# Kernel optimization log

Hardware: AMD Instinct MI355X
Metric: run time of the kernel (lower is better)

## Reference

```python
import jax, jax.numpy as jnp
import numpy as np

NUM_CLIP_VIT_FEAT = 576  # default kwarg of mixed_mask


def _mixed_mask(pad_ends, full_starts, full_ends, bt2i, blm, B, S):
    # Faithful translation of OmniAttentionMechanism.mixed_mask evaluated over
    # all (b, q_idx, kv_idx). Note python operator precedence: & binds tighter
    # than ^, so the original expression is (A&t2i) ^ (B&C&lm) ^ (D&mmu).
    q_idx = jnp.arange(S)[:, None]          # [S,1]
    kv_idx = jnp.arange(S)[None, :]         # [1,S]
    causal_qk = q_idx >= kv_idx             # [S,S]
    # kv_idx < pad_ends[b, kv_idx]  ->  arange(S) < pad_ends  (per batch row)
    pad_region = jnp.arange(S) < pad_ends   # [B,S] over kv
    causal = (~pad_region)[:, None, :] & causal_qk[None]              # [B,S,S]
    # full block: kv in [full_starts[q], full_ends[q])
    full = (kv_idx < full_ends[:, None]) & (kv_idx >= full_starts[:, None])  # [S,S]
    eye = q_idx == kv_idx                                             # [S,S]
    t2i = eye[None] ^ (causal | full[None])                           # [B,S,S]
    lm = causal_qk                                                    # [S,S]
    mmu = causal_qk | (kv_idx <= NUM_CLIP_VIT_FEAT + 3)               # [S,S]
    b = jnp.arange(B)[:, None, None]
    mask = ((b < bt2i) & t2i) \
         ^ ((b >= bt2i) & (b < bt2i + blm) & lm[None]) \
         ^ ((b >= bt2i + blm) & mmu[None])
    return mask  # [B,S,S] bool


def setup_inputs() -> dict:
    key = jax.random.key(0)
    B_T2I, B_LM, B_MMU = 4, 4, 4
    B, H, S, D = B_T2I + B_LM + B_MMU, 8, 1024, 64
    k1, k2, k3 = jax.random.split(key, 3)
    q = jax.random.normal(k1, (B, H, S, D), jnp.float32)
    k = jax.random.normal(k2, (B, H, S, D), jnp.float32)
    v = jax.random.normal(k3, (B, H, S, D), jnp.float32)

    # full_starts/full_ends from image_begin_ends=[(512,1024)]
    full_starts = np.arange(S)
    full_ends = np.arange(S)
    for ib, ie in [(512, 1024)]:
        full_starts[ib:ie] = ib
        full_ends[ib:ie] = ie

    # pad_ends from default pad_begin_ends=[(0,256),(0,300),(0,400),(0,0)]
    pad_ends = np.tile(np.arange(S), (B, 1))
    for cnt, (pb, pe) in enumerate([(0, 256), (0, 300), (0, 400), (0, 0)]):
        pad_ends[cnt, pb:pe] = pe

    return {
        "q": q, "k": k, "v": v,
        "pad_ends": jnp.asarray(pad_ends, jnp.int32),
        "full_starts": jnp.asarray(full_starts, jnp.int32),
        "full_ends": jnp.asarray(full_ends, jnp.int32),
        "batch_size_t2i": B_T2I,
        "batch_size_lm": B_LM,
    }


def reference(q, k, v, pad_ends, full_starts, full_ends, batch_size_t2i, batch_size_lm):
    B, H, S, D = q.shape
    mask = _mixed_mask(pad_ends, full_starts, full_ends,
                       batch_size_t2i, batch_size_lm, B, S)      # [B,S,S]
    scale = 1.0 / jnp.sqrt(jnp.asarray(D, q.dtype))
    scores = jnp.einsum('bhqd,bhkd->bhqk', q, k) * scale          # [B,H,S,S]
    scores = jnp.where(mask[:, None], scores, jnp.asarray(-1e30, scores.dtype))
    attn = jax.nn.softmax(scores, axis=-1)
    return jnp.einsum('bhqk,bhkd->bhqd', attn, v)
```

## Files before the change

kernel.cpp:

```cpp
#include <hip/hip_runtime.h>


typedef __attribute__((ext_vector_type(8))) short short8;
typedef __attribute__((ext_vector_type(4))) float floatx4;
typedef __attribute__((ext_vector_type(4))) unsigned int uint4v;

#define S_LEN 1024
#define D_DIM 64
#define H_NUM 8
#define B_NUM 12
#define BT2I_CONST 4
#define BLM_CONST 4
#define NUM_CLIP_P3 579
#define KV_ELEMS (B_NUM * H_NUM * S_LEN * D_DIM)
#define P_EPS 7.888609052210118e-31f

__device__ __forceinline__ float bf2f(short s) {
    unsigned int u = ((unsigned int)(unsigned short)s) << 16;
    return __builtin_bit_cast(float, u);
}
__device__ __forceinline__ short f2bf(float f) {
    unsigned int u = __builtin_bit_cast(unsigned int, f);
    unsigned int r = (u + 0x7fffu + ((u >> 16) & 1u)) >> 16;
    return (short)(unsigned short)r;
}
__device__ __forceinline__ short scale_bf(short x) {
    float f = bf2f(x) * 0.125f;
    return (short)(unsigned short)(__builtin_bit_cast(unsigned int, f) >> 16);
}
__device__ __forceinline__ int detect_bf16(const unsigned int* q) {
    int l = threadIdx.x & 63;
    unsigned int w = q[l];
    unsigned int e = (w >> 7) & 0xffu;
    bool sane = (e >= 100u && e <= 140u);
    unsigned long long m = __ballot(sane);
    return (__popcll(m) > 32) ? 1 : 0;
}

__global__ __launch_bounds__(256)
void preprocess_kv(const void* __restrict__ Kv, const void* __restrict__ Vv,
                   const unsigned int* __restrict__ Qw,
                   short* __restrict__ Kf, short* __restrict__ Vf) {
    __shared__ __align__(16) short Ls[64][72];
    const int is_bf16 = detect_bf16(Qw);
    const int x = blockIdx.x;
    const int kind = x & 1;
    const int kt = (x >> 1) & 15;
    const int bh = x >> 5;
    const int t = threadIdx.x;
    const long long base = (long long)bh * S_LEN * D_DIM + (long long)kt * 64 * D_DIM;
    const void* Src = kind ? Vv : Kv;

    #pragma unroll
    for (int j = 0; j < 4; ++j) {
        int lin = j * 1024 + t * 4;
        int row = lin >> 6, col = lin & 63;
        long long src = base + (long long)row * D_DIM + col;
        if (is_bf16) {
            const short* p = (const short*)Src + src;
            Ls[row][col] = p[0]; Ls[row][col + 1] = p[1];
            Ls[row][col + 2] = p[2]; Ls[row][col + 3] = p[3];
        } else {
            floatx4 f = *(const floatx4*)((const float*)Src + src);
            Ls[row][col] = f2bf(f[0]); Ls[row][col + 1] = f2bf(f[1]);
            Ls[row][col + 2] = f2bf(f[2]); Ls[row][col + 3] = f2bf(f[3]);
        }
    }
    __syncthreads();

    short* dst = (kind ? Vf : Kf) + ((long long)bh * 16 + kt) * 4096;
    if (kind == 0) {
        #pragma unroll
        for (int rep = 0; rep < 2; ++rep) {
            int idx = rep * 256 + t;
            int fh = idx >> 6, lam = idx & 63;
            int f = fh >> 1, hh = fh & 1, q = lam >> 4, l16 = lam & 15;
            short8 v = *(const short8*)&Ls[f * 16 + l16][hh * 32 + q * 8];
            *(short8*)(dst + (fh * 64 + lam) * 8) = v;
        }
    } else {
        #pragma unroll
        for (int rep = 0; rep < 2; ++rep) {
            int idx = rep * 256 + t;
            int ch = idx >> 6, lam = idx & 63;
            int c = ch >> 1, hh = ch & 1, q = lam >> 4, l16 = lam & 15;
            short tmp[8];
            #pragma unroll
            for (int j = 0; j < 8; ++j) tmp[j] = Ls[hh * 32 + q * 8 + j][c * 16 + l16];
            *(short8*)(dst + (ch * 64 + lam) * 8) = *(short8*)tmp;
        }
    }
}

__global__ __launch_bounds__(256, 2)
void omni_attn_main(const void* __restrict__ Qv, const int* __restrict__ pad_ends,
                    const int* __restrict__ fstarts, const int* __restrict__ fends,
                    const short* __restrict__ Kf, const short* __restrict__ Vf,
                    float* __restrict__ Out) {
    __shared__ unsigned int padbits[32];

    const int lid = blockIdx.x;
    const int h = lid & 7;
    const int perm = lid >> 3;
    const int b = perm >> 3;
    const int j = perm & 7;
    const int lpt[8] = {7, 0, 6, 1, 5, 2, 4, 3};
    const int qtb = lpt[j];
    const int qb0 = qtb * 128;

    const int t = threadIdx.x;
    const int wq = t >> 6;
    const int l = t & 63;
    const int lane16 = l & 15;
    const int quad = l >> 4;

    const int is_bf16 = detect_bf16((const unsigned int*)Qv);
    const int cls = (b < BT2I_CONST) ? 0 : ((b < BT2I_CONST + BLM_CONST) ? 1 : 2);
    const int bh = b * H_NUM + h;
    const long long base = (long long)bh * S_LEN * D_DIM;

    #pragma unroll
    for (int kk2 = 0; kk2 < 4; ++kk2) {
        int k = kk2 * 256 + t;
        bool nonpad = (k >= pad_ends[b * S_LEN + k]);
        unsigned long long m = __ballot(nonpad);
        if (l == 0) {
            int widx = kk2 * 8 + wq * 2;
            padbits[widx]     = (unsigned int)m;
            padbits[widx + 1] = (unsigned int)(m >> 32);
        }
    }
    __syncthreads();

    int fs_min, fe_max, fnp;
    {
        int fsv = min(fstarts[qb0 + l], fstarts[qb0 + 64 + l]);
        int fev = max(fends[qb0 + l],   fends[qb0 + 64 + l]);
        unsigned int word = 0u;
        if (l < 32) word = padbits[l];
        int pos = word ? (l * 32 + __builtin_ctz(word)) : 0x7fffffff;
        #pragma unroll
        for (int off = 1; off < 64; off <<= 1) {
            fsv = min(fsv, __shfl_xor(fsv, off, 64));
            fev = max(fev, __shfl_xor(fev, off, 64));
            pos = min(pos, __shfl_xor(pos, off, 64));
        }
        fs_min = fsv; fe_max = fev; fnp = pos;
    }
    const int qmax_blk = qb0 + 127;
    const bool risky = (cls == 0) && (fnp >= qb0) && (fnp <= qmax_blk);

    unsigned int keepmask = 0u;
    #pragma unroll
    for (int kt = 0; kt < 16; ++kt) {
        const int kvbase = kt * 64;
        const unsigned int w0 = padbits[kt * 2], w1 = padbits[kt * 2 + 1];
        bool keep;
        if (cls == 0) {
            bool allpad = (w0 | w1) == 0u;
            keep = risky ||
                   ((kvbase < fe_max) && (kvbase + 64 > fs_min)) ||
                   ((kvbase <= qmax_blk) && (!allpad || (kvbase >= qb0)));
        } else if (cls == 1) {
            keep = (kvbase <= qmax_blk);
        } else {
            keep = (kvbase <= qmax_blk) || (kvbase <= NUM_CLIP_P3);
        }
        keepmask |= (keep ? 1u : 0u) << kt;
    }

    short8 aq[2][2];
    #pragma unroll
    for (int rb = 0; rb < 2; ++rb) {
        const int row = qb0 + wq * 32 + rb * 16 + lane16;
        if (is_bf16) {
            const short8* qp = (const short8*)((const short*)Qv + base
                                               + (long long)row * D_DIM + quad * 8);
            short8 r0 = qp[0], r1 = qp[4];
            #pragma unroll
            for (int jj = 0; jj < 8; ++jj) {
                aq[rb][0][jj] = scale_bf(r0[jj]);
                aq[rb][1][jj] = scale_bf(r1[jj]);
            }
        } else {
            const floatx4* qp = (const floatx4*)((const float*)Qv + base
                                                 + (long long)row * D_DIM + quad * 8);
            floatx4 f0 = qp[0], f1 = qp[1], f2 = qp[8], f3 = qp[9];
            #pragma unroll
            for (int jj = 0; jj < 4; ++jj) {
                aq[rb][0][jj]     = f2bf(f0[jj] * 0.125f);
                aq[rb][0][4 + jj] = f2bf(f1[jj] * 0.125f);
                aq[rb][1][jj]     = f2bf(f2[jj] * 0.125f);
                aq[rb][1][4 + jj] = f2bf(f3[jj] * 0.125f);
            }
        }
    }

    int qvl[2], fsl[2], fel[2], fsmax[2], femin[2];
    #pragma unroll
    for (int rb = 0; rb < 2; ++rb) {
        qvl[rb] = qb0 + wq * 32 + rb * 16 + lane16;
        fsl[rb] = fstarts[qvl[rb]];
        fel[rb] = fends[qvl[rb]];
        int a = fsl[rb], e = fel[rb];
        #pragma unroll
        for (int off = 1; off < 16; off <<= 1) {
            a = max(a, __shfl_xor(a, off, 64));
            e = min(e, __shfl_xor(e, off, 64));
        }
        fsmax[rb] = a; femin[rb] = e;
    }

    floatx4 Oc[2][4];
    float lsum[2] = {0.f, 0.f};
    #pragma unroll
    for (int rb = 0; rb < 2; ++rb)
        #pragma unroll
        for (int c = 0; c < 4; ++c) Oc[rb][c] = (floatx4){0.f, 0.f, 0.f, 0.f};

    const short* Kfb = Kf + (long long)bh * (16 * 4096);
    const short* Vfb = Vf + (long long)bh * (16 * 4096);

    short8 kkf[4][2];
    short8 vvf[4][2];

    auto load_K = [&](int kt) {
        const short8* p = (const short8*)(Kfb + (long long)kt * 4096);
        #pragma unroll
        for (int f = 0; f < 4; ++f)
            #pragma unroll
            for (int hh = 0; hh < 2; ++hh)
                kkf[f][hh] = p[(f * 2 + hh) * 64 + l];
    };
    auto load_V = [&](int kt) {
        const short8* p = (const short8*)(Vfb + (long long)kt * 4096);
        #pragma unroll
        for (int c = 0; c < 4; ++c)
            #pragma unroll
            for (int hh = 0; hh < 2; ++hh)
                vvf[c][hh] = p[(c * 2 + hh) * 64 + l];
    };

    unsigned int mrem = keepmask;
    int kt = __builtin_ctz(mrem); mrem &= mrem - 1;
    load_K(kt); load_V(kt);
    for (;;) {
        int ktN = -1;
        if (mrem) { ktN = __builtin_ctz(mrem); mrem &= mrem - 1; }

        const int kvbase = kt * 64;
        const unsigned int w0c = padbits[kt * 2], w1c = padbits[kt * 2 + 1];

        short8 pa[2][2];
        #pragma unroll
        for (int rb = 0; rb < 2; ++rb) {
            floatx4 sc[4];
            #pragma unroll
            for (int f = 0; f < 4; ++f) {
                floatx4 c = (floatx4){0.f, 0.f, 0.f, 0.f};
                c = __builtin_amdgcn_mfma_f32_16x16x32_bf16(kkf[f][0], aq[rb][0], c, 0, 0, 0);
                c = __builtin_amdgcn_mfma_f32_16x16x32_bf16(kkf[f][1], aq[rb][1], c, 0, 0, 0);
                sc[f] = c;
            }
            const int qlo = qb0 + wq * 32 + rb * 16;
            bool fast;
            if (cls == 0) {
                bool np_all  = ((w0c & w1c) == 0xffffffffu);
                bool below   = (kvbase + 63 < qlo);
                bool eyefree = below || (kvbase > qlo + 15);
                fast = (np_all && below) ||
                       (eyefree && (kvbase >= fsmax[rb]) && (kvbase + 64 <= femin[rb]));
            } else if (cls == 1) {
                fast = (kvbase + 63 <= qlo);
            } else {
                fast = (kvbase + 63 <= qlo) || (kvbase + 63 <= NUM_CLIP_P3);
            }
            if (!fast) {
                const int q = qvl[rb];
                #pragma unroll
                for (int f = 0; f < 4; ++f) {
                    const unsigned int word = (f < 2) ? w0c : w1c;
                    const int sh = 16 * (f & 1) + 4 * quad;
                    #pragma unroll
                    for (int r = 0; r < 4; ++r) {
                        const int k = kvbase + f * 16 + 4 * quad + r;
                        bool m;
                        if (cls == 0) {
                            bool knp    = ((word >> (sh + r)) & 1u) != 0u;
                            bool causal = knp && (q >= k);
                            bool full   = (k >= fsl[rb]) && (k < fel[rb]);
                            m = (q == k) != (causal || full);
                        } else if (cls == 1) {
                            m = (q >= k);
                        } else {
                            m = (q >= k) || (k <= NUM_CLIP_P3);
                        }
                        sc[f][r] = m ? sc[f][r] : -1e30f;
                    }
                }
            }
            unsigned int uu[4][2];
            float ls = 0.f;
            #pragma unroll
            for (int f = 0; f < 4; ++f) {
                float p0 = __expf(sc[f][0]) + P_EPS;
                float p1 = __expf(sc[f][1]) + P_EPS;
                float p2 = __expf(sc[f][2]) + P_EPS;
                float p3 = __expf(sc[f][3]) + P_EPS;
                ls += p0 + p1 + p2 + p3;
                asm("v_cvt_pk_bf16_f32 %0, %1, %2" : "=v"(uu[f][0]) : "v"(p0), "v"(p1));
                asm("v_cvt_pk_bf16_f32 %0, %1, %2" : "=v"(uu[f][1]) : "v"(p2), "v"(p3));
            }
            lsum[rb] += ls;
            #pragma unroll
            for (int hh = 0; hh < 2; ++hh) {
                unsigned int x0 = uu[2 * hh][0],     y0 = uu[2 * hh + 1][0];
                unsigned int x1 = uu[2 * hh][1],     y1 = uu[2 * hh + 1][1];
                asm("v_permlane32_swap_b32 %0, %1" : "+v"(x0), "+v"(y0));
                asm("v_permlane16_swap_b32 %0, %1" : "+v"(x0), "+v"(y0));
                asm("v_permlane32_swap_b32 %0, %1" : "+v"(x1), "+v"(y1));
                asm("v_permlane16_swap_b32 %0, %1" : "+v"(x1), "+v"(y1));
                uint4v w;
                w[0] = x0; w[1] = x1; w[2] = y0; w[3] = y1;
                pa[rb][hh] = __builtin_bit_cast(short8, w);
            }
        }

        if (ktN >= 0) load_K(ktN);

        #pragma unroll
        for (int c = 0; c < 4; ++c) {
            Oc[0][c] = __builtin_amdgcn_mfma_f32_16x16x32_bf16(pa[0][0], vvf[c][0], Oc[0][c], 0, 0, 0);
            Oc[0][c] = __builtin_amdgcn_mfma_f32_16x16x32_bf16(pa[0][1], vvf[c][1], Oc[0][c], 0, 0, 0);
            Oc[1][c] = __builtin_amdgcn_mfma_f32_16x16x32_bf16(pa[1][0], vvf[c][0], Oc[1][c], 0, 0, 0);
            Oc[1][c] = __builtin_amdgcn_mfma_f32_16x16x32_bf16(pa[1][1], vvf[c][1], Oc[1][c], 0, 0, 0);
        }

        if (ktN >= 0) load_V(ktN);
        if (ktN < 0) break;
        kt = ktN;
    }

    #pragma unroll
    for (int rb = 0; rb < 2; ++rb) {
        float s = lsum[rb];
        s += __shfl_xor(s, 16, 64);
        s += __shfl_xor(s, 32, 64);
        float* ob = Out + ((long long)bh * S_LEN + qb0 + wq * 32 + rb * 16) * D_DIM;
        #pragma unroll
        for (int r = 0; r < 4; ++r) {
            float sv = __shfl(s, quad * 4 + r, 64);
            float inv = 1.0f / sv;
            #pragma unroll
            for (int c = 0; c < 4; ++c)
                ob[(quad * 4 + r) * D_DIM + c * 16 + lane16] = Oc[rb][c][r] * inv;
        }
    }
}

__global__ __launch_bounds__(256)
void omni_attn_fallback(const void* __restrict__ Qv, const void* __restrict__ Kv,
                        const void* __restrict__ Vv, const int* __restrict__ pad_ends,
                        const int* __restrict__ fstarts, const int* __restrict__ fends,
                        float* __restrict__ Out) {
    __shared__ short Ks[64][72];
    __shared__ short Vts[64][72];
    __shared__ short Ps[4][16][72];
    __shared__ int   padv[64];
    const int qt = blockIdx.x, h = blockIdx.y, b = blockIdx.z;
    const int t = threadIdx.x, wq = t >> 6, l = t & 63;
    const int lane16 = l & 15, quad = l >> 4;
    const int is_bf16 = detect_bf16((const unsigned int*)Qv);
    const int cls = (b < BT2I_CONST) ? 0 : ((b < BT2I_CONST + BLM_CONST) ? 1 : 2);
    const int bh = b * H_NUM + h;
    const long long base = (long long)bh * S_LEN * D_DIM;
    const short* Kb16 = (const short*)Kv + base;
    const short* Vb16 = (const short*)Vv + base;
    const float* Kbf = (const float*)Kv + base;
    const float* Vbf = (const float*)Vv + base;
    const int qbase = qt * 64 + wq * 16;
    short8 aq0, aq1;
    if (is_bf16) {
        const short8* qp = (const short8*)((const short*)Qv + base + (qbase + lane16) * D_DIM + quad * 8);
        short8 r0 = qp[0], r1 = qp[4];
        #pragma unroll
        for (int jj = 0; jj < 8; ++jj) { aq0[jj] = scale_bf(r0[jj]); aq1[jj] = scale_bf(r1[jj]); }
    } else {
        const floatx4* qp = (const floatx4*)((const float*)Qv + base + (qbase + lane16) * D_DIM + quad * 8);
        floatx4 f0 = qp[0], f1 = qp[1], f2 = qp[8], f3 = qp[9];
        #pragma unroll
        for (int jj = 0; jj < 4; ++jj) {
            aq0[jj] = f2bf(f0[jj] * 0.125f); aq0[4 + jj] = f2bf(f1[jj] * 0.125f);
            aq1[jj] = f2bf(f2[jj] * 0.125f); aq1[4 + jj] = f2bf(f3[jj] * 0.125f);
        }
    }
    int qg[4], fs[4], fe[4];
    #pragma unroll
    for (int r = 0; r < 4; ++r) {
        qg[r] = qbase + quad * 4 + r; fs[r] = fstarts[qg[r]]; fe[r] = fends[qg[r]];
    }
    floatx4 Oc[4];
    #pragma unroll
    for (int c = 0; c < 4; ++c) Oc[c] = (floatx4){0.f, 0.f, 0.f, 0.f};
    float m_i[4] = {-1e30f, -1e30f, -1e30f, -1e30f};
    float l_i[4] = {0.f, 0.f, 0.f, 0.f};
    for (int kt = 0; kt < S_LEN / 64; ++kt) {
        const int kvbase = kt * 64;
        __syncthreads();
        {
            const int kvr = t >> 2, seg = t & 3;
            if (is_bf16) {
                const short8* gk = (const short8*)(Kb16 + (kvbase + kvr) * D_DIM);
                *(short8*)&Ks[kvr][seg * 8] = gk[seg];
                *(short8*)&Ks[kvr][(seg + 4) * 8] = gk[seg + 4];
                const short8* gv = (const short8*)(Vb16 + (kvbase + kvr) * D_DIM);
                short8 v0 = gv[seg], v1 = gv[seg + 4];
                #pragma unroll
                for (int jj = 0; jj < 8; ++jj) {
                    Vts[seg * 8 + jj][kvr] = v0[jj];
                    Vts[32 + seg * 8 + jj][kvr] = v1[jj];
                }
            } else {
                const floatx4* gk = (const floatx4*)(Kbf + (kvbase + kvr) * D_DIM);
                floatx4 k0 = gk[seg * 2], k1 = gk[seg * 2 + 1];
                floatx4 k2 = gk[8 + seg * 2], k3 = gk[8 + seg * 2 + 1];
                #pragma unroll
                for (int jj = 0; jj < 4; ++jj) {
                    Ks[kvr][seg * 8 + jj] = f2bf(k0[jj]);
                    Ks[kvr][seg * 8 + 4 + jj] = f2bf(k1[jj]);
                    Ks[kvr][32 + seg * 8 + jj] = f2bf(k2[jj]);
                    Ks[kvr][32 + seg * 8 + 4 + jj] = f2bf(k3[jj]);
                }
                const floatx4* gv = (const floatx4*)(Vbf + (kvbase + kvr) * D_DIM);
                floatx4 v0 = gv[seg * 2], v1 = gv[seg * 2 + 1];
                floatx4 v2 = gv[8 + seg * 2], v3 = gv[8 + seg * 2 + 1];
                #pragma unroll
                for (int jj = 0; jj < 4; ++jj) {
                    Vts[seg * 8 + jj][kvr] = f2bf(v0[jj]);
                    Vts[seg * 8 + 4 + jj][kvr] = f2bf(v1[jj]);
                    Vts[32 + seg * 8 + jj][kvr] = f2bf(v2[jj]);
                    Vts[32 + seg * 8 + 4 + jj][kvr] = f2bf(v3[jj]);
                }
            }
            if (t < 64) {
                int kg = kvbase + t;
                padv[t] = (kg < pad_ends[b * S_LEN + kg]) ? 1 : 0;
            }
        }
        __syncthreads();
        floatx4 sc[4];
        #pragma unroll
        for (int f = 0; f < 4; ++f) {
            short8 b0 = *(const short8*)&Ks[f * 16 + lane16][quad * 8];
            short8 b1 = *(const short8*)&Ks[f * 16 + lane16][32 + quad * 8];
            floatx4 c = (floatx4){0.f, 0.f, 0.f, 0.f};
            c = __builtin_amdgcn_mfma_f32_16x16x32_bf16(aq0, b0, c, 0, 0, 0);
            c = __builtin_amdgcn_mfma_f32_16x16x32_bf16(aq1, b1, c, 0, 0, 0);
            sc[f] = c;
        }
        int col[4], cpad[4];
        #pragma unroll
        for (int f = 0; f < 4; ++f) {
            col[f] = kvbase + f * 16 + lane16;
            cpad[f] = padv[f * 16 + lane16];
        }
        if (cls == 0) {
            #pragma unroll
            for (int r = 0; r < 4; ++r) {
                const int q = qg[r];
                #pragma unroll
                for (int f = 0; f < 4; ++f) {
                    const int k = col[f];
                    bool causal = (!cpad[f]) && (q >= k);
                    bool full = (k >= fs[r]) && (k < fe[r]);
                    bool m = (q == k) != (causal || full);
                    sc[f][r] = m ? sc[f][r] : -1e30f;
                }
            }
        } else if (cls == 1) {
            #pragma unroll
            for (int r = 0; r < 4; ++r) {
                const int q = qg[r];
                #pragma unroll
                for (int f = 0; f < 4; ++f)
                    sc[f][r] = (q >= col[f]) ? sc[f][r] : -1e30f;
            }
        } else {
            #pragma unroll
            for (int r = 0; r < 4; ++r) {
                const int q = qg[r];
                #pragma unroll
                for (int f = 0; f < 4; ++f) {
                    bool m = (q >= col[f]) || (col[f] <= NUM_CLIP_P3);
                    sc[f][r] = m ? sc[f][r] : -1e30f;
                }
            }
        }
        #pragma unroll
        for (int r = 0; r < 4; ++r) {
            float rmax = fmaxf(fmaxf(sc[0][r], sc[1][r]), fmaxf(sc[2][r], sc[3][r]));
            #pragma unroll
            for (int off = 1; off < 16; off <<= 1)
                rmax = fmaxf(rmax, __shfl_xor(rmax, off, 64));
            float mnew = fmaxf(m_i[r], rmax);
            float alpha = __expf(m_i[r] - mnew);
            m_i[r] = mnew;
            float psum = 0.f;
            #pragma unroll
            for (int f = 0; f < 4; ++f) {
                float p = __expf(sc[f][r] - mnew);
                sc[f][r] = p; psum += p;
            }
            #pragma unroll
            for (int off = 1; off < 16; off <<= 1)
                psum += __shfl_xor(psum, off, 64);
            l_i[r] = l_i[r] * alpha + psum;
            Oc[0][r] *= alpha; Oc[1][r] *= alpha; Oc[2][r] *= alpha; Oc[3][r] *= alpha;
        }
        #pragma unroll
        for (int r = 0; r < 4; ++r)
            #pragma unroll
            for (int f = 0; f < 4; ++f)
                Ps[wq][quad * 4 + r][f * 16 + lane16] = f2bf(sc[f][r]);
        __syncthreads();
        short8 a0 = *(const short8*)&Ps[wq][lane16][quad * 8];
        short8 a1 = *(const short8*)&Ps[wq][lane16][32 + quad * 8];
        #pragma unroll
        for (int c = 0; c < 4; ++c) {
            short8 b0 = *(const short8*)&Vts[c * 16 + lane16][quad * 8];
            short8 b1 = *(const short8*)&Vts[c * 16 + lane16][32 + quad * 8];
            Oc[c] = __builtin_amdgcn_mfma_f32_16x16x32_bf16(a0, b0, Oc[c], 0, 0, 0);
            Oc[c] = __builtin_amdgcn_mfma_f32_16x16x32_bf16(a1, b1, Oc[c], 0, 0, 0);
        }
    }
    float* ob = Out + ((long long)bh * S_LEN + qbase) * D_DIM;
    #pragma unroll
    for (int r = 0; r < 4; ++r) {
        float inv = 1.0f / l_i[r];
        #pragma unroll
        for (int c = 0; c < 4; ++c)
            ob[(quad * 4 + r) * D_DIM + c * 16 + lane16] = Oc[c][r] * inv;
    }
}

extern "C" void kernel_launch(void* const* d_in, const int* in_sizes, int n_in,
                              void* d_out, int out_size, void* d_ws, size_t ws_size,
                              hipStream_t stream) {
    const void* Q = d_in[0];
    const void* K = d_in[1];
    const void* V = d_in[2];
    const int* pad_ends = (const int*)d_in[3];
    const int* fstarts  = (const int*)d_in[4];
    const int* fends    = (const int*)d_in[5];
    float* Out = (float*)d_out;

    const size_t need = 2 * (size_t)KV_ELEMS * 2;

    if (ws_size >= need) {
        short* Kf = (short*)d_ws;
        short* Vf = Kf + KV_ELEMS;
        preprocess_kv<<<3072, 256, 0, stream>>>(K, V, (const unsigned int*)Q, Kf, Vf);
        omni_attn_main<<<768, 256, 0, stream>>>(Q, pad_ends, fstarts, fends,
                                                Kf, Vf, Out);
    } else {
        dim3 grid(S_LEN / 64, H_NUM, B_NUM);
        omni_attn_fallback<<<grid, 256, 0, stream>>>(Q, K, V, pad_ends, fstarts,
                                                     fends, Out);
    }
}
```

Baseline: 180.1 us.

## Split attention into single-wave 32-row blocks with per-wave pad masks

The main kernel now launches 3072 single-wavefront blocks of 32 query rows instead of 768 four-wave blocks of 128 rows. The shared-memory pad bitmap and its block barrier are removed; each wave builds the pad information with ballots and recomputes the per-tile mask inline, prefetching the next tile's pad_ends. Query tiles are rotated per batch for load balance, and the keep test is loosened to match the smaller row range. The V transpose in preprocessing moves into the LDS write so both K and V share one read path. The intent is finer-grained tile skipping and better balance across CUs. The cost is that each K/V tile is reloaded by four times as many blocks, with no sharing across waves.

```diff
diff --git a/kernel.cpp b/kernel.cpp
--- a/kernel.cpp
+++ b/kernel.cpp
@@ -56,60 +56,48 @@
         int lin = j * 1024 + t * 4;
         int row = lin >> 6, col = lin & 63;
         long long src = base + (long long)row * D_DIM + col;
+        short v0, v1, v2, v3;
         if (is_bf16) {
             const short* p = (const short*)Src + src;
-            Ls[row][col] = p[0]; Ls[row][col + 1] = p[1];
-            Ls[row][col + 2] = p[2]; Ls[row][col + 3] = p[3];
+            v0 = p[0]; v1 = p[1]; v2 = p[2]; v3 = p[3];
         } else {
             floatx4 f = *(const floatx4*)((const float*)Src + src);
-            Ls[row][col] = f2bf(f[0]); Ls[row][col + 1] = f2bf(f[1]);
-            Ls[row][col + 2] = f2bf(f[2]); Ls[row][col + 3] = f2bf(f[3]);
+            v0 = f2bf(f[0]); v1 = f2bf(f[1]); v2 = f2bf(f[2]); v3 = f2bf(f[3]);
+        }
+        if (kind == 0) {
+            Ls[row][col] = v0; Ls[row][col + 1] = v1;
+            Ls[row][col + 2] = v2; Ls[row][col + 3] = v3;
+        } else {
+            Ls[col][row] = v0; Ls[col + 1][row] = v1;
+            Ls[col + 2][row] = v2; Ls[col + 3][row] = v3;
         }
     }
     __syncthreads();
 
     short* dst = (kind ? Vf : Kf) + ((long long)bh * 16 + kt) * 4096;
-    if (kind == 0) {
-        #pragma unroll
-        for (int rep = 0; rep < 2; ++rep) {
-            int idx = rep * 256 + t;
-            int fh = idx >> 6, lam = idx & 63;
-            int f = fh >> 1, hh = fh & 1, q = lam >> 4, l16 = lam & 15;
-            short8 v = *(const short8*)&Ls[f * 16 + l16][hh * 32 + q * 8];
-            *(short8*)(dst + (fh * 64 + lam) * 8) = v;
-        }
-    } else {
-        #pragma unroll
-        for (int rep = 0; rep < 2; ++rep) {
-            int idx = rep * 256 + t;
-            int ch = idx >> 6, lam = idx & 63;
-            int c = ch >> 1, hh = ch & 1, q = lam >> 4, l16 = lam & 15;
-            short tmp[8];
-            #pragma unroll
-            for (int j = 0; j < 8; ++j) tmp[j] = Ls[hh * 32 + q * 8 + j][c * 16 + l16];
-            *(short8*)(dst + (ch * 64 + lam) * 8) = *(short8*)tmp;
-        }
-    }
-}
-
-__global__ __launch_bounds__(256, 2)
+    #pragma unroll
+    for (int rep = 0; rep < 2; ++rep) {
+        int idx = rep * 256 + t;
+        int g = idx >> 6, lam = idx & 63;
+        int gg = g >> 1, hh = g & 1, q = lam >> 4, l16 = lam & 15;
+        short8 v = *(const short8*)&Ls[gg * 16 + l16][hh * 32 + q * 8];
+        *(short8*)(dst + (g * 64 + lam) * 8) = v;
+    }
+}
+
+__global__ __launch_bounds__(64, 4)
 void omni_attn_main(const void* __restrict__ Qv, const int* __restrict__ pad_ends,
                     const int* __restrict__ fstarts, const int* __restrict__ fends,
                     const short* __restrict__ Kf, const short* __restrict__ Vf,
                     float* __restrict__ Out) {
-    __shared__ unsigned int padbits[32];
-
     const int lid = blockIdx.x;
     const int h = lid & 7;
-    const int perm = lid >> 3;
-    const int b = perm >> 3;
-    const int j = perm & 7;
-    const int lpt[8] = {7, 0, 6, 1, 5, 2, 4, 3};
-    const int qtb = lpt[j];
-    const int qb0 = qtb * 128;
+    const int s = lid >> 3;
+    const int b = s >> 5;
+    const int qu = (s + 3 * b) & 31;
+    const int qb0 = qu * 32;
 
     const int t = threadIdx.x;
-    const int wq = t >> 6;
     const int l = t & 63;
     const int lane16 = l & 15;
     const int quad = l >> 4;
@@ -118,49 +106,45 @@
     const int cls = (b < BT2I_CONST) ? 0 : ((b < BT2I_CONST + BLM_CONST) ? 1 : 2);
     const int bh = b * H_NUM + h;
     const long long base = (long long)bh * S_LEN * D_DIM;
-
-    #pragma unroll
-    for (int kk2 = 0; kk2 < 4; ++kk2) {
-        int k = kk2 * 256 + t;
-        bool nonpad = (k >= pad_ends[b * S_LEN + k]);
-        unsigned long long m = __ballot(nonpad);
-        if (l == 0) {
-            int widx = kk2 * 8 + wq * 2;
-            padbits[widx]     = (unsigned int)m;
-            padbits[widx + 1] = (unsigned int)(m >> 32);
-        }
-    }
-    __syncthreads();
-
-    int fs_min, fe_max, fnp;
+    const int qmax_blk = qb0 + 31;
+
+    unsigned int apmask = 0u;
+    int fnp = 0x7fffffff;
+    if (cls == 0) {
+        #pragma unroll
+        for (int kt = 0; kt < 16; ++kt) {
+            int kg = kt * 64 + l;
+            bool nonpad = (kg >= pad_ends[b * S_LEN + kg]);
+            unsigned long long m = __ballot(nonpad);
+            apmask |= (m == 0ull ? 1u : 0u) << kt;
+            int cand = m ? (kt * 64 + __builtin_ctzll(m)) : 0x7fffffff;
+            fnp = min(fnp, cand);
+        }
+    }
+    const bool risky = (cls == 0) && (fnp >= qb0) && (fnp <= qmax_blk);
+
+    int fs_min, fe_max;
     {
-        int fsv = min(fstarts[qb0 + l], fstarts[qb0 + 64 + l]);
-        int fev = max(fends[qb0 + l],   fends[qb0 + 64 + l]);
-        unsigned int word = 0u;
-        if (l < 32) word = padbits[l];
-        int pos = word ? (l * 32 + __builtin_ctz(word)) : 0x7fffffff;
+        int fsv = fstarts[qb0 + (l & 31)];
+        int fev = fends[qb0 + (l & 31)];
         #pragma unroll
         for (int off = 1; off < 64; off <<= 1) {
             fsv = min(fsv, __shfl_xor(fsv, off, 64));
             fev = max(fev, __shfl_xor(fev, off, 64));
-            pos = min(pos, __shfl_xor(pos, off, 64));
-        }
-        fs_min = fsv; fe_max = fev; fnp = pos;
-    }
-    const int qmax_blk = qb0 + 127;
-    const bool risky = (cls == 0) && (fnp >= qb0) && (fnp <= qmax_blk);
+        }
+        fs_min = fsv; fe_max = fev;
+    }
 
     unsigned int keepmask = 0u;
     #pragma unroll
     for (int kt = 0; kt < 16; ++kt) {
         const int kvbase = kt * 64;
-        const unsigned int w0 = padbits[kt * 2], w1 = padbits[kt * 2 + 1];
         bool keep;
         if (cls == 0) {
-            bool allpad = (w0 | w1) == 0u;
+            bool allpad = ((apmask >> kt) & 1u) != 0u;
             keep = risky ||
                    ((kvbase < fe_max) && (kvbase + 64 > fs_min)) ||
-                   ((kvbase <= qmax_blk) && (!allpad || (kvbase >= qb0)));
+                   ((kvbase <= qmax_blk) && (!allpad || (kvbase + 63 >= qb0)));
         } else if (cls == 1) {
             keep = (kvbase <= qmax_blk);
         } else {
@@ -172,7 +156,7 @@
     short8 aq[2][2];
     #pragma unroll
     for (int rb = 0; rb < 2; ++rb) {
-        const int row = qb0 + wq * 32 + rb * 16 + lane16;
+        const int row = qb0 + rb * 16 + lane16;
         if (is_bf16) {
             const short8* qp = (const short8*)((const short*)Qv + base
                                                + (long long)row * D_DIM + quad * 8);
@@ -199,7 +183,7 @@
     int qvl[2], fsl[2], fel[2], fsmax[2], femin[2];
     #pragma unroll
     for (int rb = 0; rb < 2; ++rb) {
-        qvl[rb] = qb0 + wq * 32 + rb * 16 + lane16;
+        qvl[rb] = qb0 + rb * 16 + lane16;
         fsl[rb] = fstarts[qvl[rb]];
         fel[rb] = fends[qvl[rb]];
         int a = fsl[rb], e = fel[rb];
@@ -244,12 +228,18 @@
     unsigned int mrem = keepmask;
     int kt = __builtin_ctz(mrem); mrem &= mrem - 1;
     load_K(kt); load_V(kt);
+    int pev = 0;
+    if (cls == 0) pev = pad_ends[b * S_LEN + kt * 64 + l];
     for (;;) {
         int ktN = -1;
         if (mrem) { ktN = __builtin_ctz(mrem); mrem &= mrem - 1; }
 
         const int kvbase = kt * 64;
-        const unsigned int w0c = padbits[kt * 2], w1c = padbits[kt * 2 + 1];
+        unsigned long long pm = 0ull;
+        if (cls == 0) {
+            pm = __ballot((kvbase + l) >= pev);
+            if (ktN >= 0) pev = pad_ends[b * S_LEN + ktN * 64 + l];
+        }
 
         short8 pa[2][2];
         #pragma unroll
@@ -262,10 +252,10 @@
                 c = __builtin_amdgcn_mfma_f32_16x16x32_bf16(kkf[f][1], aq[rb][1], c, 0, 0, 0);
                 sc[f] = c;
             }
-            const int qlo = qb0 + wq * 32 + rb * 16;
+            const int qlo = qb0 + rb * 16;
             bool fast;
             if (cls == 0) {
-                bool np_all  = ((w0c & w1c) == 0xffffffffu);
+                bool np_all  = (pm == ~0ull);
                 bool below   = (kvbase + 63 < qlo);
                 bool eyefree = below || (kvbase > qlo + 15);
                 fast = (np_all && below) ||
@@ -279,14 +269,12 @@
                 const int q = qvl[rb];
                 #pragma unroll
                 for (int f = 0; f < 4; ++f) {
-                    const unsigned int word = (f < 2) ? w0c : w1c;
-                    const int sh = 16 * (f & 1) + 4 * quad;
                     #pragma unroll
                     for (int r = 0; r < 4; ++r) {
                         const int k = kvbase + f * 16 + 4 * quad + r;
                         bool m;
                         if (cls == 0) {
-                            bool knp    = ((word >> (sh + r)) & 1u) != 0u;
+                            bool knp    = ((pm >> (f * 16 + 4 * quad + r)) & 1ull) != 0ull;
                             bool causal = knp && (q >= k);
                             bool full   = (k >= fsl[rb]) && (k < fel[rb]);
                             m = (q == k) != (causal || full);
@@ -343,13 +331,13 @@
 
     #pragma unroll
     for (int rb = 0; rb < 2; ++rb) {
-        float s = lsum[rb];
-        s += __shfl_xor(s, 16, 64);
-        s += __shfl_xor(s, 32, 64);
-        float* ob = Out + ((long long)bh * S_LEN + qb0 + wq * 32 + rb * 16) * D_DIM;
+        float sv0 = lsum[rb];
+        sv0 += __shfl_xor(sv0, 16, 64);
+        sv0 += __shfl_xor(sv0, 32, 64);
+        float* ob = Out + ((long long)bh * S_LEN + qb0 + rb * 16) * D_DIM;
         #pragma unroll
         for (int r = 0; r < 4; ++r) {
-            float sv = __shfl(s, quad * 4 + r, 64);
+            float sv = __shfl(sv0, quad * 4 + r, 64);
             float inv = 1.0f / sv;
             #pragma unroll
             for (int c = 0; c < 4; ++c)
@@ -560,7 +548,7 @@
         short* Kf = (short*)d_ws;
         short* Vf = Kf + KV_ELEMS;
         preprocess_kv<<<3072, 256, 0, stream>>>(K, V, (const unsigned int*)Q, Kf, Vf);
-        omni_attn_main<<<768, 256, 0, stream>>>(Q, pad_ends, fstarts, fends,
+        omni_attn_main<<<3072, 64, 0, stream>>>(Q, pad_ends, fstarts, fends,
                                                 Kf, Vf, Out);
     } else {
         dim3 grid(S_LEN / 64, H_NUM, B_NUM);
```

New measurement: 383.0 us. +112.7%, slower.
